# Optimization experiments

Hardware: AMD Instinct MI355X
Metric: run time of the kernel (lower is better)

Reference implementation:

```python
import jax, jax.numpy as jnp
import numpy as np

B, S, E = 2, 2048, 2048
NH, NKV, HD = 16, 4, 128
ROPE_BASE = 10000.0
WINDOW = max(1, S // 2)


def _rotate_half(x):
    x1, x2 = jnp.split(x, 2, axis=-1)
    return jnp.concatenate([-x2, x1], axis=-1)


def setup_inputs() -> dict:
    key = jax.random.key(0)
    ks = jax.random.split(key, 6)
    x = jax.random.normal(ks[0], (B, S, E), dtype=jnp.float32)
    Wq = jax.random.normal(ks[1], (NH * HD, E), dtype=jnp.float32) * 0.02
    Wk = jax.random.normal(ks[2], (NKV * HD, E), dtype=jnp.float32) * 0.02
    Wv = jax.random.normal(ks[3], (NKV * HD, E), dtype=jnp.float32) * 0.02
    Wo = jax.random.normal(ks[4], (E, E), dtype=jnp.float32) * 0.02
    # RoPE tables, duplicated-half layout matching _rotate_half
    inv_freq = 1.0 / (ROPE_BASE ** (jnp.arange(0, HD, 2, dtype=jnp.float32) / HD))
    angles = jnp.arange(S, dtype=jnp.float32)[:, None] * inv_freq[None, :]  # [S, HD/2]
    emb = jnp.concatenate([angles, angles], axis=-1)  # [S, HD]
    cos = jnp.cos(emb)[:, None, :]  # [S, 1, HD] -> broadcasts over heads
    sin = jnp.sin(emb)[:, None, :]
    return {"x": x, "cos": cos, "sin": sin, "Wq": Wq, "Wk": Wk, "Wv": Wv, "Wo": Wo}


def reference(x, cos, sin, Wq, Wk, Wv, Wo):
    b, s, _ = x.shape
    q = (x @ Wq.T).reshape(b, s, NH, HD)
    k = (x @ Wk.T).reshape(b, s, NKV, HD)
    v = (x @ Wv.T).reshape(b, s, NKV, HD)
    # rotary (cos/sin broadcast [S,1,HD] over batch/heads)
    q = q * cos + _rotate_half(q) * sin
    k = k * cos + _rotate_half(k) * sin
    # GQA expand: repeat_interleave over head dim
    factor = NH // NKV
    k = jnp.repeat(k, factor, axis=2)  # [b,s,NH,HD]
    v = jnp.repeat(v, factor, axis=2)
    # local causal mask: 0 <= (i - j) < window
    pos = jnp.arange(s)
    dist = pos[:, None] - pos[None, :]
    mask = (dist >= 0) & (dist < WINDOW)  # [S,S]
    scale = 1.0 / jnp.sqrt(jnp.asarray(HD, dtype=x.dtype))
    scores = jnp.einsum("bqhd,bkhd->bhqk", q, k) * scale
    scores = jnp.where(mask[None, None, :, :], scores, jnp.asarray(-1e30, dtype=scores.dtype))
    attn = jax.nn.softmax(scores, axis=-1)
    out = jnp.einsum("bhqk,bkhd->bqhd", attn, v)
    out = out.reshape(b, s, NH * HD)
    return out @ Wo.T
```

## Files before the change

### kernel.cpp

```cpp
#include <hip/hip_runtime.h>

#define S_LEN 2048
#define EMB 2048
#define NH 16
#define NKV 4
#define HD 128
#define WINDOW 1024
#define BATCH 2

typedef _Float16 half8 __attribute__((ext_vector_type(8)));
typedef _Float16 half4 __attribute__((ext_vector_type(4)));
typedef float f32x4 __attribute__((ext_vector_type(4)));

#define MFMA16(a, b, c) __builtin_amdgcn_mfma_f32_16x16x32_f16((a), (b), (c), 0, 0, 0)

__device__ __forceinline__ void gload16(const void* g, void* l) {
  __builtin_amdgcn_global_load_lds(
      (const __attribute__((address_space(1))) unsigned int*)g,
      (__attribute__((address_space(3))) unsigned int*)l, 16, 0, 0);
}

__global__ __launch_bounds__(256)
void convert_all(const float* __restrict__ x, const float* __restrict__ wq,
                 const float* __restrict__ wk, const float* __restrict__ wv,
                 const float* __restrict__ wo, _Float16* __restrict__ dst) {
  size_t i = (size_t)blockIdx.x * 256 + threadIdx.x;
  const float* src; size_t u; size_t dbase;
  if (i < 1048576)      { src = x;  u = i;           dbase = 0; }
  else if (i < 1572864) { src = wq; u = i - 1048576; dbase = 8388608; }
  else if (i < 1703936) { src = wk; u = i - 1572864; dbase = 12582912; }
  else if (i < 1835008) { src = wv; u = i - 1703936; dbase = 13631488; }
  else                  { src = wo; u = i - 1835008; dbase = 14680064; }
  f32x4 a = *(const f32x4*)(src + u * 8);
  f32x4 b = *(const f32x4*)(src + u * 8 + 4);
  half8 h = { (_Float16)a[0], (_Float16)a[1], (_Float16)a[2], (_Float16)a[3],
              (_Float16)b[0], (_Float16)b[1], (_Float16)b[2], (_Float16)b[3] };
  *(half8*)(dst + dbase + u * 8) = h;
}

__global__ __launch_bounds__(256)
void qkv_gemm(const _Float16* __restrict__ x16, const _Float16* __restrict__ Wq16,
              const _Float16* __restrict__ Wk16, const _Float16* __restrict__ Wv16,
              _Float16* __restrict__ Qh, _Float16* __restrict__ Kr,
              _Float16* __restrict__ Vh) {
  __shared__ _Float16 Asm[128 * 64];
  __shared__ _Float16 Bsm[128 * 64];
  const int K = EMB;
  int m0 = blockIdx.y * 128, n0 = blockIdx.x * 128;
  const _Float16* Wp; int c0, sel;
  if (n0 < 2048)      { Wp = Wq16; c0 = n0;        sel = 0; }
  else if (n0 < 2560) { Wp = Wk16; c0 = n0 - 2048; sel = 1; }
  else                { Wp = Wv16; c0 = n0 - 2560; sel = 2; }

  int t = threadIdx.x, lane = t & 63, w = t >> 6;
  int l15 = lane & 15, quad = lane >> 4;
  int wm = (w >> 1) * 64, wn = (w & 1) * 64;
  int srow = t >> 3;
  int cg = (t & 7) ^ (srow & 7);

  f32x4 acc[4][4] = {};
  for (int kt = 0; kt < K; kt += 64) {
    __syncthreads();
#pragma unroll
    for (int p = 0; p < 4; ++p) {
      int row = p * 32 + srow;
      gload16(x16 + (size_t)(m0 + row) * K + kt + cg * 8, (char*)Asm + p * 4096 + t * 16);
      gload16(Wp + (size_t)(c0 + row) * K + kt + cg * 8, (char*)Bsm + p * 4096 + t * 16);
    }
    __syncthreads();
#pragma unroll
    for (int kc = 0; kc < 2; ++kc) {
      half8 af[4], bf[4];
#pragma unroll
      for (int i = 0; i < 4; ++i) {
        int row = wm + i * 16 + l15;
        af[i] = *(const half8*)&Asm[row * 64 + (((kc * 4 + quad) ^ (row & 7)) * 8)];
      }
#pragma unroll
      for (int i = 0; i < 4; ++i) {
        int row = wn + i * 16 + l15;
        bf[i] = *(const half8*)&Bsm[row * 64 + (((kc * 4 + quad) ^ (row & 7)) * 8)];
      }
#pragma unroll
      for (int mi = 0; mi < 4; ++mi)
#pragma unroll
        for (int ni = 0; ni < 4; ++ni)
          acc[mi][ni] = MFMA16(af[mi], bf[ni], acc[mi][ni]);
    }
  }
#pragma unroll
  for (int mi = 0; mi < 4; ++mi)
#pragma unroll
    for (int ni = 0; ni < 4; ++ni)
#pragma unroll
      for (int r = 0; r < 4; ++r) {
        int row = m0 + wm + mi * 16 + quad * 4 + r;
        int col = c0 + wn + ni * 16 + l15;
        _Float16 val = (_Float16)acc[mi][ni][r];
        if (sel == 0) {
          Qh[(size_t)row * 2048 + col] = val;
        } else {
          int b = row >> 11, s = row & 2047, kvh = col >> 7, d = col & 127;
          size_t o = ((size_t)(b * NKV + kvh) * S_LEN + s) * HD + d;
          if (sel == 1) Kr[o] = val; else Vh[o] = val;
        }
      }
}

__global__ __launch_bounds__(256)
void rope_k(_Float16* __restrict__ Kr, const float* __restrict__ cosT,
            const float* __restrict__ sinT) {
  int t = threadIdx.x;
  int row = blockIdx.x * 32 + (t >> 3);
  int s = row & (S_LEN - 1);
  int d0 = (t & 7) * 8;
  _Float16* p = Kr + (size_t)row * HD;
  half8 lo = *(half8*)(p + d0);
  half8 hi = *(half8*)(p + d0 + 64);
  float cv[8], sv[8];
  *(f32x4*)&cv[0] = *(const f32x4*)(cosT + (size_t)s * HD + d0);
  *(f32x4*)&cv[4] = *(const f32x4*)(cosT + (size_t)s * HD + d0 + 4);
  *(f32x4*)&sv[0] = *(const f32x4*)(sinT + (size_t)s * HD + d0);
  *(f32x4*)&sv[4] = *(const f32x4*)(sinT + (size_t)s * HD + d0 + 4);
  half8 rlo, rhi;
#pragma unroll
  for (int u = 0; u < 8; ++u) {
    float l = (float)lo[u], h = (float)hi[u];
    rlo[u] = (_Float16)(l * cv[u] - h * sv[u]);
    rhi[u] = (_Float16)(h * cv[u] + l * sv[u]);
  }
  *(half8*)(p + d0) = rlo;
  *(half8*)(p + d0 + 64) = rhi;
}

__global__ __launch_bounds__(256)
void transpose_v(const _Float16* __restrict__ Vh, _Float16* __restrict__ Vt) {
  __shared__ _Float16 Tm[64 * 72];
  int t = threadIdx.x;
  int s0 = blockIdx.x * 64, d0 = blockIdx.y * 64;
  size_t plane = (size_t)blockIdx.z * S_LEN * HD;
#pragma unroll
  for (int it = 0; it < 2; ++it) {
    int chunk = t + 256 * it;
    int r = chunk >> 3, c8 = chunk & 7;
    *(half8*)&Tm[r * 72 + c8 * 8] =
        *(const half8*)(Vh + plane + (size_t)(s0 + r) * HD + d0 + c8 * 8);
  }
  __syncthreads();
#pragma unroll
  for (int it = 0; it < 2; ++it) {
    int chunk = t + 256 * it;
    int dr = chunk >> 3, sc8 = chunk & 7;
    half8 v;
#pragma unroll
    for (int j = 0; j < 8; ++j) v[j] = Tm[(sc8 * 8 + j) * 72 + dr];
    *(half8*)(Vt + plane + (size_t)(d0 + dr) * S_LEN + s0 + sc8 * 8) = v;
  }
}

__global__ __launch_bounds__(256, 2)
void attn_fused(const _Float16* Qh, const _Float16* __restrict__ Kr,
                const _Float16* __restrict__ Vt, const float* __restrict__ cosT,
                const float* __restrict__ sinT, _Float16* Oh) {
  const float SL2E = 0.08838834764831843f * 1.4426950408889634f;
  int c = blockIdx.x & 255, half = blockIdx.x >> 8;
  int h = c & 15, j = c >> 4;
  int qt = half ? (15 - j) : j;
  int b = half;
  int kvh = h >> 2;
  int q0 = qt * 128;
  int t = threadIdx.x, lane = t & 63, w = t >> 6;
  int l15 = lane & 15, quad = lane >> 4;

  __shared__ _Float16 Ksm[64 * 128];
  __shared__ _Float16 Vsm[128 * 64];
  __shared__ _Float16 Psm[4][2][16 * 68];

  int qw0 = q0 + w * 32;

  half8 qf[2][4];
#pragma unroll
  for (int g = 0; g < 2; ++g) {
    int qi = qw0 + g * 16 + l15;
    const _Float16* qrow = Qh + (size_t)(b * S_LEN + qi) * EMB + h * HD;
    const float* crow = cosT + (size_t)qi * HD;
    const float* srow = sinT + (size_t)qi * HD;
    float qv[4][8], cv[2][8], sv[2][8];
#pragma unroll
    for (int kc = 0; kc < 4; ++kc) {
      half8 q8 = *(const half8*)(qrow + kc * 32 + quad * 8);
#pragma unroll
      for (int jj = 0; jj < 8; ++jj) qv[kc][jj] = (float)q8[jj];
    }
#pragma unroll
    for (int kc = 0; kc < 2; ++kc) {
      int d0 = kc * 32 + quad * 8;
      *(f32x4*)&cv[kc][0] = *(const f32x4*)(crow + d0);
      *(f32x4*)&cv[kc][4] = *(const f32x4*)(crow + d0 + 4);
      *(f32x4*)&sv[kc][0] = *(const f32x4*)(srow + d0);
      *(f32x4*)&sv[kc][4] = *(const f32x4*)(srow + d0 + 4);
    }
#pragma unroll
    for (int kc = 0; kc < 4; ++kc)
#pragma unroll
      for (int jj = 0; jj < 8; ++jj) {
        float rot = (kc < 2) ? -qv[kc + 2][jj] : qv[kc - 2][jj];
        qf[g][kc][jj] = (_Float16)((qv[kc][jj] * cv[kc & 1][jj] + rot * sv[kc & 1][jj]) * SL2E);
      }
  }

  const _Float16* khead = Kr + (size_t)(b * NKV + kvh) * S_LEN * HD;
  const _Float16* vhead = Vt + (size_t)(b * NKV + kvh) * HD * S_LEN;

  f32x4 oacc[2][8] = {};
  float l_r[2] = {0.f, 0.f};

  int kt_lo = (q0 >= WINDOW) ? ((q0 - (WINDOW - 1)) >> 6) : 0;
  int kt_hi = qt * 2 + 1;
  for (int kt = kt_lo; kt <= kt_hi; ++kt) {
    int k0 = kt * 64;

    if (kt > kt_lo) __syncthreads();
#pragma unroll
    for (int i = 0; i < 4; ++i) {
      int u = t + 256 * i;
      int r = u >> 4, cc = u & 15;
      gload16(khead + (((size_t)(k0 + r)) << 7) + ((cc ^ (r & 15)) << 3),
              (char*)Ksm + (size_t)u * 16);
    }
#pragma unroll
    for (int i = 0; i < 4; ++i) {
      int u = t + 256 * i;
      int d = u >> 3, cc = u & 7;
      gload16(vhead + (((size_t)d) << 11) + k0 + ((cc ^ (d & 7)) << 3),
              (char*)Vsm + (size_t)u * 16);
    }
    __syncthreads();

    f32x4 sfr[2][4];
#pragma unroll
    for (int nb = 0; nb < 4; ++nb) {
      int r = nb * 16 + l15;
      half8 kf[4];
#pragma unroll
      for (int dc = 0; dc < 4; ++dc) {
        int cw = dc * 4 + quad;
        kf[dc] = *(const half8*)&Ksm[r * 128 + ((cw ^ l15) << 3)];
      }
      f32x4 s0 = {0.f, 0.f, 0.f, 0.f}, s1 = {0.f, 0.f, 0.f, 0.f};
#pragma unroll
      for (int dc = 0; dc < 4; ++dc) {
        s0 = MFMA16(kf[dc], qf[0][dc], s0);
        s1 = MFMA16(kf[dc], qf[1][dc], s1);
      }
      sfr[0][nb] = s0; sfr[1][nb] = s1;
    }

#pragma unroll
    for (int g = 0; g < 2; ++g) {
      int qi = qw0 + g * 16 + l15;
#pragma unroll
      for (int nb = 0; nb < 4; ++nb) {
        half4 ph;
#pragma unroll
        for (int r = 0; r < 4; ++r) {
          int key = k0 + nb * 16 + quad * 4 + r;
          int dd = qi - key;
          float sv = (dd >= 0 && dd < WINDOW) ? sfr[g][nb][r] : -1e4f;
          float p = __builtin_amdgcn_exp2f(fminf(sv, 14.0f));
          l_r[g] += p;
          ph[r] = (_Float16)p;
        }
        *(half4*)&Psm[w][g][l15 * 68 + nb * 16 + quad * 4] = ph;
      }
    }

    half8 pf[2][2];
#pragma unroll
    for (int g = 0; g < 2; ++g) {
      pf[g][0] = *(const half8*)&Psm[w][g][l15 * 68 + quad * 8];
      pf[g][1] = *(const half8*)&Psm[w][g][l15 * 68 + 32 + quad * 8];
    }

#pragma unroll
    for (int nc = 0; nc < 8; ++nc) {
      int d = nc * 16 + l15;
      half8 v0 = *(const half8*)&Vsm[d * 64 + (((quad) ^ (d & 7)) << 3)];
      half8 v1 = *(const half8*)&Vsm[d * 64 + (((4 + quad) ^ (d & 7)) << 3)];
      oacc[0][nc] = MFMA16(v0, pf[0][0], oacc[0][nc]);
      oacc[0][nc] = MFMA16(v1, pf[0][1], oacc[0][nc]);
      oacc[1][nc] = MFMA16(v0, pf[1][0], oacc[1][nc]);
      oacc[1][nc] = MFMA16(v1, pf[1][1], oacc[1][nc]);
    }
  }

#pragma unroll
  for (int g = 0; g < 2; ++g) {
    float lr = l_r[g];
    lr += __shfl_xor(lr, 16, 64);
    lr += __shfl_xor(lr, 32, 64);
    float inv = 1.0f / lr;
    int qi = qw0 + g * 16 + l15;
    _Float16* orow = Oh + (size_t)(b * S_LEN + qi) * EMB + h * HD;
#pragma unroll
    for (int nc = 0; nc < 8; ++nc) {
      half4 o4;
#pragma unroll
      for (int r = 0; r < 4; ++r) o4[r] = (_Float16)(oacc[g][nc][r] * inv);
      *(half4*)&orow[nc * 16 + quad * 4] = o4;
    }
  }
}

__global__ __launch_bounds__(256)
void out_gemm(const _Float16* __restrict__ A, const _Float16* __restrict__ B,
              float* __restrict__ out) {
  __shared__ _Float16 Asm[128 * 64];
  __shared__ _Float16 Bsm[128 * 64];
  const int K = EMB;
  int m0 = blockIdx.y * 128, n0 = blockIdx.x * 128;
  int t = threadIdx.x, lane = t & 63, w = t >> 6;
  int l15 = lane & 15, quad = lane >> 4;
  int wm = (w >> 1) * 64, wn = (w & 1) * 64;
  int srow = t >> 3;
  int cg = (t & 7) ^ (srow & 7);
  f32x4 acc[4][4] = {};
  for (int kt = 0; kt < K; kt += 64) {
    __syncthreads();
#pragma unroll
    for (int p = 0; p < 4; ++p) {
      int row = p * 32 + srow;
      gload16(A + (size_t)(m0 + row) * K + kt + cg * 8, (char*)Asm + p * 4096 + t * 16);
      gload16(B + (size_t)(n0 + row) * K + kt + cg * 8, (char*)Bsm + p * 4096 + t * 16);
    }
    __syncthreads();
#pragma unroll
    for (int kc = 0; kc < 2; ++kc) {
      half8 af[4], bf[4];
#pragma unroll
      for (int i = 0; i < 4; ++i) {
        int row = wm + i * 16 + l15;
        af[i] = *(const half8*)&Asm[row * 64 + (((kc * 4 + quad) ^ (row & 7)) * 8)];
      }
#pragma unroll
      for (int i = 0; i < 4; ++i) {
        int row = wn + i * 16 + l15;
        bf[i] = *(const half8*)&Bsm[row * 64 + (((kc * 4 + quad) ^ (row & 7)) * 8)];
      }
#pragma unroll
      for (int mi = 0; mi < 4; ++mi)
#pragma unroll
        for (int ni = 0; ni < 4; ++ni)
          acc[mi][ni] = MFMA16(af[mi], bf[ni], acc[mi][ni]);
    }
  }
#pragma unroll
  for (int mi = 0; mi < 4; ++mi)
#pragma unroll
    for (int ni = 0; ni < 4; ++ni)
#pragma unroll
      for (int r = 0; r < 4; ++r) {
        int row = m0 + wm + mi * 16 + quad * 4 + r;
        int col = n0 + wn + ni * 16 + l15;
        out[(size_t)row * EMB + col] = acc[mi][ni][r];
      }
}

extern "C" void kernel_launch(void* const* d_in, const int* in_sizes, int n_in,
                              void* d_out, int out_size, void* d_ws, size_t ws_size,
                              hipStream_t stream) {
  const float* x    = (const float*)d_in[0];
  const float* cosT = (const float*)d_in[1];
  const float* sinT = (const float*)d_in[2];
  const float* Wq   = (const float*)d_in[3];
  const float* Wk   = (const float*)d_in[4];
  const float* Wv   = (const float*)d_in[5];
  const float* Wo   = (const float*)d_in[6];
  float* out = (float*)d_out;

  char* ws = (char*)d_ws;
  _Float16* x16  = (_Float16*)(ws);
  _Float16* Wq16 = (_Float16*)(ws + 16777216);
  _Float16* Wk16 = (_Float16*)(ws + 25165824);
  _Float16* Wv16 = (_Float16*)(ws + 27262976);
  _Float16* Wo16 = (_Float16*)(ws + 29360128);
  _Float16* Qh   = (_Float16*)(ws + 37748736);
  _Float16* Kr   = (_Float16*)(ws + 54525952);
  _Float16* Vh   = (_Float16*)(ws + 58720256);
  _Float16* Vt   = x16;
  _Float16* Oh   = Qh;

  convert_all<<<dim3(9216), 256, 0, stream>>>(x, Wq, Wk, Wv, Wo, (_Float16*)ws);
  qkv_gemm<<<dim3(24, 32), 256, 0, stream>>>(x16, Wq16, Wk16, Wv16, Qh, Kr, Vh);
  rope_k<<<dim3(512), 256, 0, stream>>>(Kr, cosT, sinT);
  transpose_v<<<dim3(32, 2, 8), 256, 0, stream>>>(Vh, Vt);
  attn_fused<<<dim3(512), 256, 0, stream>>>(Qh, Kr, Vt, cosT, sinT, Oh);
  out_gemm<<<dim3(16, 32), 256, 0, stream>>>(Oh, Wo16, out);
}
```

Baseline: 300.5 us.

## Double-buffer LDS loads in GEMMs and attention, fuse V transpose into QKV epilogue

Both GEMMs now use a two-stage LDS ring with a K-tile of 32 instead of a single 64-wide buffer. The next tile's global-to-LDS load is issued before computing the current one, so there is one barrier per iteration instead of two. Attention gets the same K/V double buffering, plus a P staging layout chosen so each lane reads its half8 fragment contiguously. The separate V transpose kernel is removed: QKV GEMM writes V directly in [d][s] order, trading a kernel launch and an extra pass for strided scalar stores. Doubled LDS in attention may limit occupancy at the 2-block launch bound.

```diff
diff --git a/kernel.cpp b/kernel.cpp
--- a/kernel.cpp
+++ b/kernel.cpp
@@ -42,9 +42,9 @@
 void qkv_gemm(const _Float16* __restrict__ x16, const _Float16* __restrict__ Wq16,
               const _Float16* __restrict__ Wk16, const _Float16* __restrict__ Wv16,
               _Float16* __restrict__ Qh, _Float16* __restrict__ Kr,
-              _Float16* __restrict__ Vh) {
-  __shared__ _Float16 Asm[128 * 64];
-  __shared__ _Float16 Bsm[128 * 64];
+              _Float16* __restrict__ Vt) {
+  __shared__ _Float16 Asm[2][128 * 32];
+  __shared__ _Float16 Bsm[2][128 * 32];
   const int K = EMB;
   int m0 = blockIdx.y * 128, n0 = blockIdx.x * 128;
   const _Float16* Wp; int c0, sel;
@@ -55,38 +55,39 @@
   int t = threadIdx.x, lane = t & 63, w = t >> 6;
   int l15 = lane & 15, quad = lane >> 4;
   int wm = (w >> 1) * 64, wn = (w & 1) * 64;
-  int srow = t >> 3;
-  int cg = (t & 7) ^ (srow & 7);
+
+  auto stage = [&](int kt, int p) {
+#pragma unroll
+    for (int i = 0; i < 2; ++i) {
+      int u = t + 256 * i;
+      int row = u >> 2, cc = u & 3, g = cc ^ (row & 3);
+      gload16(x16 + (size_t)(m0 + row) * K + kt + g * 8, (char*)Asm[p] + (size_t)u * 16);
+      gload16(Wp + (size_t)(c0 + row) * K + kt + g * 8, (char*)Bsm[p] + (size_t)u * 16);
+    }
+  };
 
   f32x4 acc[4][4] = {};
-  for (int kt = 0; kt < K; kt += 64) {
+  stage(0, 0);
+  for (int it = 0; it < 64; ++it) {
+    int p = it & 1;
     __syncthreads();
-#pragma unroll
-    for (int p = 0; p < 4; ++p) {
-      int row = p * 32 + srow;
-      gload16(x16 + (size_t)(m0 + row) * K + kt + cg * 8, (char*)Asm + p * 4096 + t * 16);
-      gload16(Wp + (size_t)(c0 + row) * K + kt + cg * 8, (char*)Bsm + p * 4096 + t * 16);
-    }
-    __syncthreads();
-#pragma unroll
-    for (int kc = 0; kc < 2; ++kc) {
-      half8 af[4], bf[4];
-#pragma unroll
-      for (int i = 0; i < 4; ++i) {
-        int row = wm + i * 16 + l15;
-        af[i] = *(const half8*)&Asm[row * 64 + (((kc * 4 + quad) ^ (row & 7)) * 8)];
-      }
-#pragma unroll
-      for (int i = 0; i < 4; ++i) {
-        int row = wn + i * 16 + l15;
-        bf[i] = *(const half8*)&Bsm[row * 64 + (((kc * 4 + quad) ^ (row & 7)) * 8)];
-      }
-#pragma unroll
-      for (int mi = 0; mi < 4; ++mi)
-#pragma unroll
-        for (int ni = 0; ni < 4; ++ni)
-          acc[mi][ni] = MFMA16(af[mi], bf[ni], acc[mi][ni]);
-    }
+    if (it < 63) stage((it + 1) * 32, 1 - p);
+    half8 af[4], bf[4];
+#pragma unroll
+    for (int i = 0; i < 4; ++i) {
+      int row = wm + i * 16 + l15;
+      af[i] = *(const half8*)&Asm[p][row * 32 + ((quad ^ (row & 3)) << 3)];
+    }
+#pragma unroll
+    for (int i = 0; i < 4; ++i) {
+      int row = wn + i * 16 + l15;
+      bf[i] = *(const half8*)&Bsm[p][row * 32 + ((quad ^ (row & 3)) << 3)];
+    }
+#pragma unroll
+    for (int mi = 0; mi < 4; ++mi)
+#pragma unroll
+      for (int ni = 0; ni < 4; ++ni)
+        acc[mi][ni] = MFMA16(af[mi], bf[ni], acc[mi][ni]);
   }
 #pragma unroll
   for (int mi = 0; mi < 4; ++mi)
@@ -101,8 +102,10 @@
           Qh[(size_t)row * 2048 + col] = val;
         } else {
           int b = row >> 11, s = row & 2047, kvh = col >> 7, d = col & 127;
-          size_t o = ((size_t)(b * NKV + kvh) * S_LEN + s) * HD + d;
-          if (sel == 1) Kr[o] = val; else Vh[o] = val;
+          if (sel == 1)
+            Kr[((size_t)(b * NKV + kvh) * S_LEN + s) * HD + d] = val;
+          else
+            Vt[((size_t)(b * NKV + kvh) * HD + d) * S_LEN + s] = val;
         }
       }
 }
@@ -133,31 +136,6 @@
   *(half8*)(p + d0 + 64) = rhi;
 }
 
-__global__ __launch_bounds__(256)
-void transpose_v(const _Float16* __restrict__ Vh, _Float16* __restrict__ Vt) {
-  __shared__ _Float16 Tm[64 * 72];
-  int t = threadIdx.x;
-  int s0 = blockIdx.x * 64, d0 = blockIdx.y * 64;
-  size_t plane = (size_t)blockIdx.z * S_LEN * HD;
-#pragma unroll
-  for (int it = 0; it < 2; ++it) {
-    int chunk = t + 256 * it;
-    int r = chunk >> 3, c8 = chunk & 7;
-    *(half8*)&Tm[r * 72 + c8 * 8] =
-        *(const half8*)(Vh + plane + (size_t)(s0 + r) * HD + d0 + c8 * 8);
-  }
-  __syncthreads();
-#pragma unroll
-  for (int it = 0; it < 2; ++it) {
-    int chunk = t + 256 * it;
-    int dr = chunk >> 3, sc8 = chunk & 7;
-    half8 v;
-#pragma unroll
-    for (int j = 0; j < 8; ++j) v[j] = Tm[(sc8 * 8 + j) * 72 + dr];
-    *(half8*)(Vt + plane + (size_t)(d0 + dr) * S_LEN + s0 + sc8 * 8) = v;
-  }
-}
-
 __global__ __launch_bounds__(256, 2)
 void attn_fused(const _Float16* Qh, const _Float16* __restrict__ Kr,
                 const _Float16* __restrict__ Vt, const float* __restrict__ cosT,
@@ -172,9 +150,9 @@
   int t = threadIdx.x, lane = t & 63, w = t >> 6;
   int l15 = lane & 15, quad = lane >> 4;
 
-  __shared__ _Float16 Ksm[64 * 128];
-  __shared__ _Float16 Vsm[128 * 64];
-  __shared__ _Float16 Psm[4][2][16 * 68];
+  __shared__ _Float16 Ksm[2][64 * 128];
+  __shared__ _Float16 Vsm[2][128 * 64];
+  __shared__ _Float16 PB[4][2][2][64 * 8];
 
   int qw0 = q0 + w * 32;
 
@@ -212,30 +190,36 @@
   const _Float16* khead = Kr + (size_t)(b * NKV + kvh) * S_LEN * HD;
   const _Float16* vhead = Vt + (size_t)(b * NKV + kvh) * HD * S_LEN;
 
-  f32x4 oacc[2][8] = {};
-  float l_r[2] = {0.f, 0.f};
-
-  int kt_lo = (q0 >= WINDOW) ? ((q0 - (WINDOW - 1)) >> 6) : 0;
-  int kt_hi = qt * 2 + 1;
-  for (int kt = kt_lo; kt <= kt_hi; ++kt) {
+  auto stage = [&](int kt, int p) {
     int k0 = kt * 64;
-
-    if (kt > kt_lo) __syncthreads();
 #pragma unroll
     for (int i = 0; i < 4; ++i) {
       int u = t + 256 * i;
       int r = u >> 4, cc = u & 15;
       gload16(khead + (((size_t)(k0 + r)) << 7) + ((cc ^ (r & 15)) << 3),
-              (char*)Ksm + (size_t)u * 16);
+              (char*)Ksm[p] + (size_t)u * 16);
     }
 #pragma unroll
     for (int i = 0; i < 4; ++i) {
       int u = t + 256 * i;
       int d = u >> 3, cc = u & 7;
       gload16(vhead + (((size_t)d) << 11) + k0 + ((cc ^ (d & 7)) << 3),
-              (char*)Vsm + (size_t)u * 16);
-    }
+              (char*)Vsm[p] + (size_t)u * 16);
+    }
+  };
+
+  f32x4 oacc[2][8] = {};
+  float l_r[2] = {0.f, 0.f};
+
+  int kt_lo = (q0 >= WINDOW) ? ((q0 - (WINDOW - 1)) >> 6) : 0;
+  int kt_hi = qt * 2 + 1;
+
+  stage(kt_lo, 0);
+  for (int kt = kt_lo; kt <= kt_hi; ++kt) {
+    int p = (kt - kt_lo) & 1;
+    int k0 = kt * 64;
     __syncthreads();
+    if (kt < kt_hi) stage(kt + 1, 1 - p);
 
     f32x4 sfr[2][4];
 #pragma unroll
@@ -245,7 +229,7 @@
 #pragma unroll
       for (int dc = 0; dc < 4; ++dc) {
         int cw = dc * 4 + quad;
-        kf[dc] = *(const half8*)&Ksm[r * 128 + ((cw ^ l15) << 3)];
+        kf[dc] = *(const half8*)&Ksm[p][r * 128 + ((cw ^ l15) << 3)];
       }
       f32x4 s0 = {0.f, 0.f, 0.f, 0.f}, s1 = {0.f, 0.f, 0.f, 0.f};
 #pragma unroll
@@ -267,26 +251,27 @@
           int key = k0 + nb * 16 + quad * 4 + r;
           int dd = qi - key;
           float sv = (dd >= 0 && dd < WINDOW) ? sfr[g][nb][r] : -1e4f;
-          float p = __builtin_amdgcn_exp2f(fminf(sv, 14.0f));
-          l_r[g] += p;
-          ph[r] = (_Float16)p;
+          float pv = __builtin_amdgcn_exp2f(fminf(sv, 14.0f));
+          l_r[g] += pv;
+          ph[r] = (_Float16)pv;
         }
-        *(half4*)&Psm[w][g][l15 * 68 + nb * 16 + quad * 4] = ph;
+        *(half4*)&PB[w][g][nb >> 1]
+            [((l15 + 16 * (((nb & 1) << 1) + (quad >> 1))) << 3) + ((quad & 1) << 2)] = ph;
       }
     }
 
     half8 pf[2][2];
 #pragma unroll
     for (int g = 0; g < 2; ++g) {
-      pf[g][0] = *(const half8*)&Psm[w][g][l15 * 68 + quad * 8];
-      pf[g][1] = *(const half8*)&Psm[w][g][l15 * 68 + 32 + quad * 8];
+      pf[g][0] = *(const half8*)&PB[w][g][0][lane << 3];
+      pf[g][1] = *(const half8*)&PB[w][g][1][lane << 3];
     }
 
 #pragma unroll
     for (int nc = 0; nc < 8; ++nc) {
       int d = nc * 16 + l15;
-      half8 v0 = *(const half8*)&Vsm[d * 64 + (((quad) ^ (d & 7)) << 3)];
-      half8 v1 = *(const half8*)&Vsm[d * 64 + (((4 + quad) ^ (d & 7)) << 3)];
+      half8 v0 = *(const half8*)&Vsm[p][d * 64 + ((quad ^ (d & 7)) << 3)];
+      half8 v1 = *(const half8*)&Vsm[p][d * 64 + (((4 + quad) ^ (d & 7)) << 3)];
       oacc[0][nc] = MFMA16(v0, pf[0][0], oacc[0][nc]);
       oacc[0][nc] = MFMA16(v1, pf[0][1], oacc[0][nc]);
       oacc[1][nc] = MFMA16(v0, pf[1][0], oacc[1][nc]);
@@ -315,44 +300,46 @@
 __global__ __launch_bounds__(256)
 void out_gemm(const _Float16* __restrict__ A, const _Float16* __restrict__ B,
               float* __restrict__ out) {
-  __shared__ _Float16 Asm[128 * 64];
-  __shared__ _Float16 Bsm[128 * 64];
+  __shared__ _Float16 Asm[2][128 * 32];
+  __shared__ _Float16 Bsm[2][128 * 32];
   const int K = EMB;
   int m0 = blockIdx.y * 128, n0 = blockIdx.x * 128;
   int t = threadIdx.x, lane = t & 63, w = t >> 6;
   int l15 = lane & 15, quad = lane >> 4;
   int wm = (w >> 1) * 64, wn = (w & 1) * 64;
-  int srow = t >> 3;
-  int cg = (t & 7) ^ (srow & 7);
+
+  auto stage = [&](int kt, int p) {
+#pragma unroll
+    for (int i = 0; i < 2; ++i) {
+      int u = t + 256 * i;
+      int row = u >> 2, cc = u & 3, g = cc ^ (row & 3);
+      gload16(A + (size_t)(m0 + row) * K + kt + g * 8, (char*)Asm[p] + (size_t)u * 16);
+      gload16(B + (size_t)(n0 + row) * K + kt + g * 8, (char*)Bsm[p] + (size_t)u * 16);
+    }
+  };
+
   f32x4 acc[4][4] = {};
-  for (int kt = 0; kt < K; kt += 64) {
+  stage(0, 0);
+  for (int it = 0; it < 64; ++it) {
+    int p = it & 1;
     __syncthreads();
-#pragma unroll
-    for (int p = 0; p < 4; ++p) {
-      int row = p * 32 + srow;
-      gload16(A + (size_t)(m0 + row) * K + kt + cg * 8, (char*)Asm + p * 4096 + t * 16);
-      gload16(B + (size_t)(n0 + row) * K + kt + cg * 8, (char*)Bsm + p * 4096 + t * 16);
-    }
-    __syncthreads();
-#pragma unroll
-    for (int kc = 0; kc < 2; ++kc) {
-      half8 af[4], bf[4];
-#pragma unroll
-      for (int i = 0; i < 4; ++i) {
-        int row = wm + i * 16 + l15;
-        af[i] = *(const half8*)&Asm[row * 64 + (((kc * 4 + quad) ^ (row & 7)) * 8)];
-      }
-#pragma unroll
-      for (int i = 0; i < 4; ++i) {
-        int row = wn + i * 16 + l15;
-        bf[i] = *(const half8*)&Bsm[row * 64 + (((kc * 4 + quad) ^ (row & 7)) * 8)];
-      }
-#pragma unroll
-      for (int mi = 0; mi < 4; ++mi)
-#pragma unroll
-        for (int ni = 0; ni < 4; ++ni)
-          acc[mi][ni] = MFMA16(af[mi], bf[ni], acc[mi][ni]);
-    }
+    if (it < 63) stage((it + 1) * 32, 1 - p);
+    half8 af[4], bf[4];
+#pragma unroll
+    for (int i = 0; i < 4; ++i) {
+      int row = wm + i * 16 + l15;
+      af[i] = *(const half8*)&Asm[p][row * 32 + ((quad ^ (row & 3)) << 3)];
+    }
+#pragma unroll
+    for (int i = 0; i < 4; ++i) {
+      int row = wn + i * 16 + l15;
+      bf[i] = *(const half8*)&Bsm[p][row * 32 + ((quad ^ (row & 3)) << 3)];
+    }
+#pragma unroll
+    for (int mi = 0; mi < 4; ++mi)
+#pragma unroll
+      for (int ni = 0; ni < 4; ++ni)
+        acc[mi][ni] = MFMA16(af[mi], bf[ni], acc[mi][ni]);
   }
 #pragma unroll
   for (int mi = 0; mi < 4; ++mi)
@@ -386,14 +373,12 @@
   _Float16* Wo16 = (_Float16*)(ws + 29360128);
   _Float16* Qh   = (_Float16*)(ws + 37748736);
   _Float16* Kr   = (_Float16*)(ws + 54525952);
-  _Float16* Vh   = (_Float16*)(ws + 58720256);
-  _Float16* Vt   = x16;
+  _Float16* Vt   = (_Float16*)(ws + 58720256);
   _Float16* Oh   = Qh;
 
   convert_all<<<dim3(9216), 256, 0, stream>>>(x, Wq, Wk, Wv, Wo, (_Float16*)ws);
-  qkv_gemm<<<dim3(24, 32), 256, 0, stream>>>(x16, Wq16, Wk16, Wv16, Qh, Kr, Vh);
+  qkv_gemm<<<dim3(24, 32), 256, 0, stream>>>(x16, Wq16, Wk16, Wv16, Qh, Kr, Vt);
   rope_k<<<dim3(512), 256, 0, stream>>>(Kr, cosT, sinT);
-  transpose_v<<<dim3(32, 2, 8), 256, 0, stream>>>(Vh, Vt);
   attn_fused<<<dim3(512), 256, 0, stream>>>(Qh, Kr, Vt, cosT, sinT, Oh);
   out_gemm<<<dim3(16, 32), 256, 0, stream>>>(Oh, Wo16, out);
 }
```

New measurement: 303.5 us. About the same (+1.0%).
